# Kernel tuning notes

Measured on AMD Instinct MI355X. Metric: run time of the kernel, lower is better.

Reference implementation:

```python
import jax, jax.numpy as jnp
import numpy as np

H = 8      # heads
D = 64     # dim_head
N0 = 1024  # modality-0 tokens
N1 = 1024  # modality-1 tokens
N = N0 + N1  # == token_num
DI = H * D   # dim_inner = 512


def setup_inputs() -> dict:
    key = jax.random.key(0)
    ks = jax.random.split(key, 10)
    s = 0.02
    return {
        "x0": jax.random.normal(ks[0], (1, N0, 512), jnp.float32),
        "x1": jax.random.normal(ks[1], (1, N1, 512), jnp.float32),
        "mask0": jnp.ones((1, N0), jnp.bool_),
        "mask1": jnp.ones((1, N1), jnp.bool_),
        "attn_dist": jax.random.normal(ks[2], (1, N, N), jnp.float32),
        "W_in0": jax.random.normal(ks[3], (512, 3 * DI), jnp.float32) * s,
        "W_in1": jax.random.normal(ks[4], (512, 3 * DI), jnp.float32) * s,
        "W_tau": jax.random.normal(ks[5], (DI, N * H), jnp.float32) * s,
        "b_tau": jax.random.normal(ks[6], (N * H,), jnp.float32) * s,
        "W_out0": jax.random.normal(ks[7], (DI, 512), jnp.float32) * s,
        "W_out1": jax.random.normal(ks[8], (DI, 512), jnp.float32) * s,
    }


def _split_heads(qkv, B, n):
    # (B, n, 3*H*D) -> (3, B, H, n, D)   [matches Rearrange 'b n (qkv h d) -> qkv b h n d']
    return qkv.reshape(B, n, 3, H, D).transpose(2, 0, 3, 1, 4)


def reference(x0, x1, mask0, mask1, attn_dist, W_in0, W_in1, W_tau, b_tau, W_out0, W_out1):
    B = x0.shape[0]
    qkv0 = _split_heads(x0 @ W_in0, B, N0)
    qkv1 = _split_heads(x1 @ W_in1, B, N1)
    qkv = jnp.concatenate([qkv0, qkv1], axis=3)  # pack along token axis -> (3,B,H,N,D)
    q, k, v = qkv[0], qkv[1], qkv[2]
    mask = jnp.concatenate([mask0, mask1], axis=1)  # (B, N)

    sim = jnp.einsum('bhid,bhjd->bhij', q, k) / jnp.sqrt(jnp.array(D, q.dtype))
    neg = -jnp.finfo(sim.dtype).max
    sim = jnp.where(mask[:, None, None, :], sim, neg)

    # taus: raw row-major reshape of q (B,H,N,D) -> (B,N,H*D), as in torch .reshape
    q_flat = q.reshape(B, N, H * D)
    taus = (q_flat @ W_tau + b_tau).reshape(B, N, N, H)
    bias = (taus * attn_dist[..., None]).transpose(0, 3, 1, 2)  # (B,H,N,N)
    sim = sim - bias

    attn = jax.nn.softmax(sim.astype(jnp.float32), axis=-1).astype(sim.dtype)
    out = jnp.einsum('bhij,bhjd->bhid', attn, v)
    out = out.transpose(0, 2, 1, 3).reshape(B, N, H * D)  # merge heads

    out0 = out[:, :N0] @ W_out0
    out1 = out[:, N0:] @ W_out1
    return (out0, out1)
```

## Files before the change

kernel.cpp:

```cpp
#include <hip/hip_runtime.h>
#include <stdint.h>

typedef __bf16 bf16;
typedef __bf16 bf16x8 __attribute__((ext_vector_type(8)));
typedef float f32x4 __attribute__((ext_vector_type(4)));
typedef unsigned short u16x8 __attribute__((ext_vector_type(8)));

#define MFMA16(a, b, c) __builtin_amdgcn_mfma_f32_16x16x32_bf16(a, b, c, 0, 0, 0)

static __device__ __forceinline__ bf16x8 lds_frag(const unsigned short* p) {
  return __builtin_bit_cast(bf16x8, *(const u16x8*)p);
}

static __device__ __forceinline__ bf16x8 gmem_frag(const bf16* p) {
  return __builtin_bit_cast(bf16x8, *(const u16x8*)p);
}

static __device__ __forceinline__ u16x8 cvt8(const float* p) {
  f32x4 a = *(const f32x4*)p;
  f32x4 b = *(const f32x4*)(p + 4);
  u16x8 r;
#pragma unroll
  for (int e = 0; e < 4; ++e) {
    r[e] = __builtin_bit_cast(unsigned short, (bf16)a[e]);
    r[4 + e] = __builtin_bit_cast(unsigned short, (bf16)b[e]);
  }
  return r;
}

__global__ __launch_bounds__(256) void prep_kernel(
    const float* __restrict__ Wti, const float* __restrict__ btau,
    const float* __restrict__ x0, const float* __restrict__ x1,
    const float* __restrict__ Win0, const float* __restrict__ Win1,
    const float* __restrict__ Wo0, const float* __restrict__ Wo1,
    bf16* __restrict__ Wto, float* __restrict__ bto, bf16* __restrict__ xb,
    bf16* __restrict__ Winb0, bf16* __restrict__ Winb1,
    bf16* __restrict__ Wob0, bf16* __restrict__ Wob1) {
  const int b = blockIdx.x;
  const int tid = threadIdx.x;
  __shared__ unsigned short shm[8 * 32 * 72];

  if (b < 512) {
    const int c0 = (b & 7) * 64;
    const int j0 = (b >> 3) * 32;
#pragma unroll
    for (int it = 0; it < 8; ++it) {
      int idx = it * 256 + tid;
      int c = idx >> 5, j = idx & 31;
      u16x8 v = cvt8(Wti + (size_t)(c0 + c) * 16384 + (j0 + j) * 8);
#pragma unroll
      for (int h = 0; h < 8; ++h) shm[(h * 32 + j) * 72 + c] = v[h];
    }
    __syncthreads();
#pragma unroll
    for (int it = 0; it < 8; ++it) {
      int chunk = it * 256 + tid;
      int row = chunk >> 3, ck = chunk & 7;
      int h = row >> 5, j = row & 31;
      u16x8 v = *(const u16x8*)&shm[row * 72 + ck * 8];
      *(u16x8*)((unsigned short*)Wto + (size_t)(h * 2048 + j0 + j) * 512 + c0 + ck * 8) = v;
    }
    if ((b & 7) == 0) {
      int j = tid >> 3, h = tid & 7;
      bto[h * 2048 + j0 + j] = btau[(j0 + j) * 8 + h];
    }
  } else if (b < 896) {
    int t = b - 512;
    const float* W = t < 192 ? Win0 : Win1;
    bf16* Wb = t < 192 ? Winb0 : Winb1;
    t = t < 192 ? t : t - 192;
    const int c0 = (t & 7) * 64, n0 = (t >> 3) * 64;
#pragma unroll
    for (int it = 0; it < 2; ++it) {
      int idx = it * 256 + tid;
      int c = idx >> 3, nn = idx & 7;
      u16x8 v = cvt8(W + (size_t)(c0 + c) * 1536 + n0 + nn * 8);
#pragma unroll
      for (int e = 0; e < 8; ++e) shm[(nn * 8 + e) * 72 + c] = v[e];
    }
    __syncthreads();
#pragma unroll
    for (int it = 0; it < 2; ++it) {
      int idx = it * 256 + tid;
      int n = idx >> 3, ck = idx & 7;
      *(u16x8*)((unsigned short*)Wb + (size_t)(n0 + n) * 512 + c0 + ck * 8) =
          *(const u16x8*)&shm[n * 72 + ck * 8];
    }
  } else if (b < 1408) {
    int t = b - 896;
    const float* src = t < 256 ? x0 : x1;
    size_t dst0 = t < 256 ? 0 : 524288;
    int tt = t < 256 ? t : t - 256;
    size_t off = (size_t)tt * 2048 + tid * 8;
    u16x8 v = cvt8(src + off);
    *(u16x8*)((unsigned short*)xb + dst0 + off) = v;
  } else {
    int t = b - 1408;
    const float* W = t < 64 ? Wo0 : Wo1;
    bf16* Wb = t < 64 ? Wob0 : Wob1;
    t &= 63;
    const int c0 = (t & 7) * 64, n0 = (t >> 3) * 64;
#pragma unroll
    for (int it = 0; it < 2; ++it) {
      int idx = it * 256 + tid;
      int c = idx >> 3, nn = idx & 7;
      u16x8 v = cvt8(W + (size_t)(c0 + c) * 512 + n0 + nn * 8);
#pragma unroll
      for (int e = 0; e < 8; ++e) shm[(nn * 8 + e) * 72 + c] = v[e];
    }
    __syncthreads();
#pragma unroll
    for (int it = 0; it < 2; ++it) {
      int idx = it * 256 + tid;
      int n = idx >> 3, ck = idx & 7;
      *(u16x8*)((unsigned short*)Wb + (size_t)(n0 + n) * 512 + c0 + ck * 8) =
          *(const u16x8*)&shm[n * 72 + ck * 8];
    }
  }
}

__global__ __launch_bounds__(256) void qkv_gemm(
    const bf16* __restrict__ xb, const bf16* __restrict__ Winb0, const bf16* __restrict__ Winb1,
    bf16* __restrict__ Qb, bf16* __restrict__ Kb, bf16* __restrict__ Vt_g) {
  const int i0 = blockIdx.x * 128, c0 = blockIdx.y * 128;
  const bf16* Bm = (i0 < 1024) ? Winb0 : Winb1;
  const int tid = threadIdx.x;
  const int lane = tid & 63, wave = tid >> 6;
  const int l16 = lane & 15, quad = lane >> 4;
  const int mrow = (wave & 1) * 64, ncol = (wave >> 1) * 64;
  __shared__ unsigned short As[128 * 64];
  __shared__ unsigned short Bs[128 * 64];
  f32x4 acc[4][4] = {};

  for (int k0 = 0; k0 < 512; k0 += 64) {
    __syncthreads();
#pragma unroll
    for (int c = 0; c < 4; ++c) {
      int s = c * 256 + tid;
      int row = s >> 3, pos = s & 7;
      int kc = pos ^ (row & 7);
      __builtin_amdgcn_global_load_lds((const unsigned int*)(xb + (size_t)(i0 + row) * 512 + k0 + kc * 8),
                                       (unsigned int*)&As[s * 8], 16, 0, 0);
      __builtin_amdgcn_global_load_lds((const unsigned int*)(Bm + (size_t)(c0 + row) * 512 + k0 + kc * 8),
                                       (unsigned int*)&Bs[s * 8], 16, 0, 0);
    }
    __syncthreads();
#pragma unroll
    for (int kb = 0; kb < 2; ++kb) {
      bf16x8 a[4], b[4];
#pragma unroll
      for (int mt = 0; mt < 4; ++mt) {
        int row = mrow + mt * 16 + l16;
        a[mt] = lds_frag(&As[row * 64 + (((kb * 4 + quad) ^ (row & 7)) * 8)]);
      }
#pragma unroll
      for (int nt = 0; nt < 4; ++nt) {
        int row = ncol + nt * 16 + l16;
        b[nt] = lds_frag(&Bs[row * 64 + (((kb * 4 + quad) ^ (row & 7)) * 8)]);
      }
#pragma unroll
      for (int mt = 0; mt < 4; ++mt)
#pragma unroll
        for (int nt = 0; nt < 4; ++nt) acc[mt][nt] = MFMA16(a[mt], b[nt], acc[mt][nt]);
    }
  }
#pragma unroll
  for (int mt = 0; mt < 4; ++mt)
#pragma unroll
    for (int nt = 0; nt < 4; ++nt)
#pragma unroll
      for (int r = 0; r < 4; ++r) {
        int row = i0 + mrow + mt * 16 + quad * 4 + r;
        int col = c0 + ncol + nt * 16 + l16;
        int qsel = col >> 9, h = (col >> 6) & 7, d = col & 63;
        bf16 val = (bf16)acc[mt][nt][r];
        if (qsel == 2) {
          Vt_g[(size_t)(h * 64 + d) * 2048 + row] = val;
        } else {
          bf16* dst = qsel == 0 ? Qb : Kb;
          dst[(size_t)(h * 2048 + row) * 64 + d] = val;
        }
      }
}

__global__ __launch_bounds__(256) void tau_gemm(
    const bf16* __restrict__ Qb, const bf16* __restrict__ Wt,
    const float* __restrict__ bt, const float* __restrict__ ad, bf16* __restrict__ T) {
  const int i0 = blockIdx.x * 128;
  const int j0 = blockIdx.y * 16;
  const int tid = threadIdx.x;
  const int lane = tid & 63, wave = tid >> 6;
  const int l16 = lane & 15, quad = lane >> 4;
  const int mrow = (wave & 1) * 64, ncol = (wave >> 1) * 64;
  __shared__ unsigned short As[128 * 128];
  __shared__ unsigned short Bs[128 * 128];
  f32x4 acc[4][4] = {};

  for (int k0 = 0; k0 < 512; k0 += 128) {
    __syncthreads();
#pragma unroll
    for (int c = 0; c < 8; ++c) {
      int s = c * 256 + tid;
      int row = s >> 4, pos = s & 15;
      int kc = pos ^ (row & 7);
      __builtin_amdgcn_global_load_lds((const unsigned int*)(Qb + (size_t)(i0 + row) * 512 + k0 + kc * 8),
                                       (unsigned int*)&As[s * 8], 16, 0, 0);
      __builtin_amdgcn_global_load_lds(
          (const unsigned int*)(Wt + (size_t)((row >> 4) * 2048 + j0 + (row & 15)) * 512 + k0 + kc * 8),
          (unsigned int*)&Bs[s * 8], 16, 0, 0);
    }
    __syncthreads();
#pragma unroll
    for (int kb = 0; kb < 4; ++kb) {
      bf16x8 a[4], b[4];
#pragma unroll
      for (int mt = 0; mt < 4; ++mt) {
        int row = mrow + mt * 16 + l16;
        a[mt] = lds_frag(&As[row * 128 + (((kb * 4 + quad) ^ (row & 7)) * 8)]);
      }
#pragma unroll
      for (int nt = 0; nt < 4; ++nt) {
        int row = ncol + nt * 16 + l16;
        b[nt] = lds_frag(&Bs[row * 128 + (((kb * 4 + quad) ^ (row & 7)) * 8)]);
      }
#pragma unroll
      for (int mt = 0; mt < 4; ++mt)
#pragma unroll
        for (int nt = 0; nt < 4; ++nt) acc[mt][nt] = MFMA16(a[mt], b[nt], acc[mt][nt]);
    }
  }
  float btv[4];
  int hh[4];
#pragma unroll
  for (int nt = 0; nt < 4; ++nt) {
    int c = ncol + nt * 16 + l16;
    hh[nt] = c >> 4;
    btv[nt] = bt[hh[nt] * 2048 + j0 + l16];
  }
#pragma unroll
  for (int mt = 0; mt < 4; ++mt)
#pragma unroll
    for (int r = 0; r < 4; ++r) {
      int row = i0 + mrow + mt * 16 + quad * 4 + r;
      float av = ad[(size_t)row * 2048 + j0 + l16];
#pragma unroll
      for (int nt = 0; nt < 4; ++nt)
        T[(size_t)hh[nt] * 4194304 + (size_t)row * 2048 + j0 + l16] =
            (bf16)((acc[mt][nt][r] + btv[nt]) * av);
    }
}

__global__ __launch_bounds__(256) void attn_kernel(
    const bf16* __restrict__ Qb, const bf16* __restrict__ Kb, const bf16* __restrict__ Vt_g,
    const bf16* __restrict__ T, float* __restrict__ Op, float* __restrict__ Ml) {
  const int h = blockIdx.y;
  const int i0 = blockIdx.x * 64;
  const int js = blockIdx.z;
  const int tid = threadIdx.x;
  const int lane = tid & 63, wave = tid >> 6;
  const int l16 = lane & 15, quad = lane >> 4;
  __shared__ unsigned short Ps[64 * 72];

  const bf16* Kh = Kb + (size_t)h * (2048 * 64);
  const bf16* Vh = Vt_g + (size_t)h * (64 * 2048);
  const bf16* Th = T + (size_t)h * (2048 * 2048);

  bf16x8 aQ[2];
#pragma unroll
  for (int kk = 0; kk < 2; ++kk)
    aQ[kk] = gmem_frag(Qb + (size_t)(h * 2048 + i0 + wave * 16 + l16) * 64 + kk * 32 + quad * 8);
  f32x4 Oacc[4] = {};
  float m_run[4], l_run[4];
#pragma unroll
  for (int r = 0; r < 4; ++r) { m_run[r] = -3.0e38f; l_run[r] = 0.f; }
  const int rowl = wave * 16 + quad * 4;

  for (int t = 0; t < 8; ++t) {
    const int j0 = js * 512 + t * 64;
    bf16x8 bk[4][2];
#pragma unroll
    for (int nt = 0; nt < 4; ++nt)
#pragma unroll
      for (int kk = 0; kk < 2; ++kk)
        bk[nt][kk] = gmem_frag(Kh + (size_t)(j0 + nt * 16 + l16) * 64 + kk * 32 + quad * 8);
    unsigned short tbu[4][4];
#pragma unroll
    for (int nt = 0; nt < 4; ++nt)
#pragma unroll
      for (int r = 0; r < 4; ++r)
        tbu[nt][r] = *((const unsigned short*)Th + (size_t)(i0 + rowl + r) * 2048 + j0 + nt * 16 + l16);

    f32x4 S[4] = {};
#pragma unroll
    for (int nt = 0; nt < 4; ++nt)
#pragma unroll
      for (int kk = 0; kk < 2; ++kk) S[nt] = MFMA16(aQ[kk], bk[nt][kk], S[nt]);

    float sv[4][4];
#pragma unroll
    for (int nt = 0; nt < 4; ++nt)
#pragma unroll
      for (int r = 0; r < 4; ++r)
        sv[nt][r] = S[nt][r] * 0.125f - (float)__builtin_bit_cast(bf16, tbu[nt][r]);

#pragma unroll
    for (int r = 0; r < 4; ++r) {
      float mx = fmaxf(fmaxf(sv[0][r], sv[1][r]), fmaxf(sv[2][r], sv[3][r]));
#pragma unroll
      for (int o = 1; o < 16; o <<= 1) mx = fmaxf(mx, __shfl_xor(mx, o, 16));
      float mnew = fmaxf(m_run[r], mx);
      float alpha = __expf(m_run[r] - mnew);
      m_run[r] = mnew;
      float rs = 0.f;
#pragma unroll
      for (int nt = 0; nt < 4; ++nt) { sv[nt][r] = __expf(sv[nt][r] - mnew); rs += sv[nt][r]; }
#pragma unroll
      for (int o = 1; o < 16; o <<= 1) rs += __shfl_xor(rs, o, 16);
      l_run[r] = l_run[r] * alpha + rs;
#pragma unroll
      for (int dt = 0; dt < 4; ++dt) Oacc[dt][r] *= alpha;
    }
#pragma unroll
    for (int nt = 0; nt < 4; ++nt)
#pragma unroll
      for (int r = 0; r < 4; ++r)
        Ps[(rowl + r) * 72 + nt * 16 + l16] =
            __builtin_bit_cast(unsigned short, (bf16)sv[nt][r]);
    __builtin_amdgcn_s_waitcnt(0xC07F);
    __builtin_amdgcn_wave_barrier();
#pragma unroll
    for (int kk = 0; kk < 2; ++kk) {
      bf16x8 aP = lds_frag(&Ps[(wave * 16 + l16) * 72 + kk * 32 + quad * 8]);
#pragma unroll
      for (int dt = 0; dt < 4; ++dt) {
        bf16x8 bv = gmem_frag(Vh + (size_t)(dt * 16 + l16) * 2048 + j0 + kk * 32 + quad * 8);
        Oacc[dt] = MFMA16(aP, bv, Oacc[dt]);
      }
    }
    __builtin_amdgcn_wave_barrier();
  }
  const size_t pb = ((size_t)js * 8 + h) * 2048;
#pragma unroll
  for (int r = 0; r < 4; ++r) {
    int rowg = i0 + rowl + r;
#pragma unroll
    for (int dt = 0; dt < 4; ++dt)
      Op[(pb + rowg) * 64 + dt * 16 + l16] = Oacc[dt][r];
    if (l16 == 0) {
      Ml[(pb + rowg) * 2 + 0] = m_run[r];
      Ml[(pb + rowg) * 2 + 1] = l_run[r];
    }
  }
}

__global__ __launch_bounds__(256) void merge_kernel(
    const float* __restrict__ Op, const float* __restrict__ Ml, bf16* __restrict__ om) {
  const int gr = blockIdx.x * 4 + (threadIdx.x >> 6);
  const int d = threadIdx.x & 63;
  float ms[4];
  float mmax = -3.0e38f;
#pragma unroll
  for (int s = 0; s < 4; ++s) {
    ms[s] = Ml[((size_t)s * 16384 + gr) * 2 + 0];
    mmax = fmaxf(mmax, ms[s]);
  }
  float lsum = 0.f, o = 0.f;
#pragma unroll
  for (int s = 0; s < 4; ++s) {
    float w = __expf(ms[s] - mmax);
    lsum += Ml[((size_t)s * 16384 + gr) * 2 + 1] * w;
    o += Op[((size_t)s * 16384 + gr) * 64 + d] * w;
  }
  int h = gr >> 11, i = gr & 2047;
  om[(size_t)i * 512 + h * 64 + d] = (bf16)(o / lsum);
}

__global__ __launch_bounds__(256) void out_proj(
    const bf16* __restrict__ om, const bf16* __restrict__ Wob0, const bf16* __restrict__ Wob1,
    float* __restrict__ out) {
  const int mod = blockIdx.z;
  const bf16* Bw = mod ? Wob1 : Wob0;
  float* outp = out + (size_t)mod * (1024 * 512);
  const int i0 = blockIdx.x * 64, c0 = blockIdx.y * 64;
  const int grow0 = mod * 1024 + i0;
  const int tid = threadIdx.x;
  const int lane = tid & 63, wave = tid >> 6;
  const int l16 = lane & 15, quad = lane >> 4;
  const int mrow = (wave & 1) * 32, ncol = (wave >> 1) * 32;
  __shared__ unsigned short As[64 * 64];
  __shared__ unsigned short Bs[64 * 64];
  f32x4 acc[2][2] = {};

  for (int k0 = 0; k0 < 512; k0 += 64) {
    __syncthreads();
#pragma unroll
    for (int c = 0; c < 2; ++c) {
      int s = c * 256 + tid;
      int row = s >> 3, pos = s & 7;
      int kc = pos ^ (row & 7);
      __builtin_amdgcn_global_load_lds((const unsigned int*)(om + (size_t)(grow0 + row) * 512 + k0 + kc * 8),
                                       (unsigned int*)&As[s * 8], 16, 0, 0);
      __builtin_amdgcn_global_load_lds((const unsigned int*)(Bw + (size_t)(c0 + row) * 512 + k0 + kc * 8),
                                       (unsigned int*)&Bs[s * 8], 16, 0, 0);
    }
    __syncthreads();
#pragma unroll
    for (int kb = 0; kb < 2; ++kb) {
      bf16x8 a[2], b[2];
#pragma unroll
      for (int mt = 0; mt < 2; ++mt) {
        int row = mrow + mt * 16 + l16;
        a[mt] = lds_frag(&As[row * 64 + (((kb * 4 + quad) ^ (row & 7)) * 8)]);
      }
#pragma unroll
      for (int nt = 0; nt < 2; ++nt) {
        int row = ncol + nt * 16 + l16;
        b[nt] = lds_frag(&Bs[row * 64 + (((kb * 4 + quad) ^ (row & 7)) * 8)]);
      }
#pragma unroll
      for (int mt = 0; mt < 2; ++mt)
#pragma unroll
        for (int nt = 0; nt < 2; ++nt) acc[mt][nt] = MFMA16(a[mt], b[nt], acc[mt][nt]);
    }
  }
#pragma unroll
  for (int mt = 0; mt < 2; ++mt)
#pragma unroll
    for (int nt = 0; nt < 2; ++nt)
#pragma unroll
      for (int r = 0; r < 4; ++r) {
        int row = i0 + mrow + mt * 16 + quad * 4 + r;
        int col = c0 + ncol + nt * 16 + l16;
        outp[(size_t)row * 512 + col] = acc[mt][nt][r];
      }
}

extern "C" void kernel_launch(void* const* d_in, const int* in_sizes, int n_in,
                              void* d_out, int out_size, void* d_ws, size_t ws_size,
                              hipStream_t stream) {
  (void)in_sizes; (void)n_in; (void)out_size; (void)ws_size;
  const float* x0   = (const float*)d_in[0];
  const float* x1   = (const float*)d_in[1];
  const float* ad   = (const float*)d_in[4];
  const float* Win0 = (const float*)d_in[5];
  const float* Win1 = (const float*)d_in[6];
  const float* Wtau = (const float*)d_in[7];
  const float* btau = (const float*)d_in[8];
  const float* Wo0  = (const float*)d_in[9];
  const float* Wo1  = (const float*)d_in[10];
  float* out = (float*)d_out;

  bf16* ws = (bf16*)d_ws;
  bf16* Qb = ws;
  bf16* Kb = Qb + 1048576;
  bf16* Vt_g = Kb + 1048576;
  bf16* Wt = Vt_g + 1048576;
  bf16* T  = Wt + 8388608;
  bf16* om = T + 33554432;
  float* bt = (float*)(om + 1048576);
  float* Ml = bt + 16384;
  bf16* Wob0 = (bf16*)(Ml + 131072);
  bf16* Wob1 = Wob0 + 262144;
  float* Op = (float*)Wt;
  bf16* xb    = T;
  bf16* Winb0 = T + 1048576;
  bf16* Winb1 = Winb0 + 786432;

  prep_kernel<<<1536, 256, 0, stream>>>(Wtau, btau, x0, x1, Win0, Win1, Wo0, Wo1,
                                        Wt, bt, xb, Winb0, Winb1, Wob0, Wob1);
  qkv_gemm<<<dim3(16, 12), 256, 0, stream>>>(xb, Winb0, Winb1, Qb, Kb, Vt_g);
  tau_gemm<<<dim3(16, 128), 256, 0, stream>>>(Qb, Wt, bt, ad, T);
  attn_kernel<<<dim3(32, 8, 4), 256, 0, stream>>>(Qb, Kb, Vt_g, T, Op, Ml);
  merge_kernel<<<4096, 256, 0, stream>>>(Op, Ml, om);
  out_proj<<<dim3(16, 8, 2), 256, 0, stream>>>(om, Wob0, Wob1, out);
}
```

Baseline: 263.8 us.

## Stage K, V and bias tiles in LDS via direct global-to-LDS loads

The attention kernel now loads each 64-wide K, V^T and bias tile into shared memory with global_load_lds, using an XOR-swizzled layout for K and V. Before, each wave fetched these straight from global memory with per-lane loads, and the bias was read as scattered 2-byte loads. The block now shares one coalesced 16-byte-per-lane copy, at the cost of two __syncthreads per iteration with no double buffering, so load latency is not overlapped with compute.

After: 231.2 us. -12.3%, faster.

```diff
diff --git a/kernel.cpp b/kernel.cpp
--- a/kernel.cpp
+++ b/kernel.cpp
@@ -259,6 +259,9 @@
   const int tid = threadIdx.x;
   const int lane = tid & 63, wave = tid >> 6;
   const int l16 = lane & 15, quad = lane >> 4;
+  __shared__ unsigned short Ks[64 * 64];
+  __shared__ unsigned short Vt[64 * 64];
+  __shared__ unsigned short Tb[64 * 64];
   __shared__ unsigned short Ps[64 * 72];
 
   const bf16* Kh = Kb + (size_t)h * (2048 * 64);
@@ -277,32 +280,42 @@
 
   for (int t = 0; t < 8; ++t) {
     const int j0 = js * 512 + t * 64;
-    bf16x8 bk[4][2];
+    __syncthreads();
+#pragma unroll
+    for (int c = 0; c < 2; ++c) {
+      int s = c * 256 + tid;
+      int r8 = s >> 3, pos = s & 7;
+      int sc = pos ^ (r8 & 7);
+      __builtin_amdgcn_global_load_lds(
+          (const unsigned int*)(Kh + (size_t)(j0 + r8) * 64 + sc * 8),
+          (unsigned int*)&Ks[s * 8], 16, 0, 0);
+      __builtin_amdgcn_global_load_lds(
+          (const unsigned int*)(Vh + (size_t)r8 * 2048 + j0 + sc * 8),
+          (unsigned int*)&Vt[s * 8], 16, 0, 0);
+      __builtin_amdgcn_global_load_lds(
+          (const unsigned int*)(Th + (size_t)(i0 + r8) * 2048 + j0 + pos * 8),
+          (unsigned int*)&Tb[s * 8], 16, 0, 0);
+    }
+    __syncthreads();
+
+    f32x4 S[4] = {};
+#pragma unroll
+    for (int nt = 0; nt < 4; ++nt) {
+      int row = nt * 16 + l16;
+#pragma unroll
+      for (int kk = 0; kk < 2; ++kk) {
+        bf16x8 bk = lds_frag(&Ks[row * 64 + (((kk * 4 + quad) ^ (row & 7)) * 8)]);
+        S[nt] = MFMA16(aQ[kk], bk, S[nt]);
+      }
+    }
+    float sv[4][4];
 #pragma unroll
     for (int nt = 0; nt < 4; ++nt)
 #pragma unroll
-      for (int kk = 0; kk < 2; ++kk)
-        bk[nt][kk] = gmem_frag(Kh + (size_t)(j0 + nt * 16 + l16) * 64 + kk * 32 + quad * 8);
-    unsigned short tbu[4][4];
-#pragma unroll
-    for (int nt = 0; nt < 4; ++nt)
-#pragma unroll
-      for (int r = 0; r < 4; ++r)
-        tbu[nt][r] = *((const unsigned short*)Th + (size_t)(i0 + rowl + r) * 2048 + j0 + nt * 16 + l16);
-
-    f32x4 S[4] = {};
-#pragma unroll
-    for (int nt = 0; nt < 4; ++nt)
-#pragma unroll
-      for (int kk = 0; kk < 2; ++kk) S[nt] = MFMA16(aQ[kk], bk[nt][kk], S[nt]);
-
-    float sv[4][4];
-#pragma unroll
-    for (int nt = 0; nt < 4; ++nt)
-#pragma unroll
-      for (int r = 0; r < 4; ++r)
-        sv[nt][r] = S[nt][r] * 0.125f - (float)__builtin_bit_cast(bf16, tbu[nt][r]);
-
+      for (int r = 0; r < 4; ++r) {
+        float tb = (float)__builtin_bit_cast(bf16, Tb[(rowl + r) * 64 + nt * 16 + l16]);
+        sv[nt][r] = S[nt][r] * 0.125f - tb;
+      }
 #pragma unroll
     for (int r = 0; r < 4; ++r) {
       float mx = fmaxf(fmaxf(sv[0][r], sv[1][r]), fmaxf(sv[2][r], sv[3][r]));
@@ -333,7 +346,8 @@
       bf16x8 aP = lds_frag(&Ps[(wave * 16 + l16) * 72 + kk * 32 + quad * 8]);
 #pragma unroll
       for (int dt = 0; dt < 4; ++dt) {
-        bf16x8 bv = gmem_frag(Vh + (size_t)(dt * 16 + l16) * 2048 + j0 + kk * 32 + quad * 8);
+        int row = dt * 16 + l16;
+        bf16x8 bv = lds_frag(&Vt[row * 64 + (((kk * 4 + quad) ^ (row & 7)) * 8)]);
         Oacc[dt] = MFMA16(aP, bv, Oacc[dt]);
       }
     }
```
